# Kernel tuning notes

Measured on AMD Instinct MI355X. Metric: run time of the kernel, lower is better.

## Reference

```python
import jax, jax.numpy as jnp
import numpy as np
from jax import lax

T = 8  # primary_vec_length


def setup_inputs() -> dict:
    key = jax.random.key(0)
    k1, k2, k3 = jax.random.split(key, 3)
    x = jax.random.normal(k1, (32, 256, 64, 64), dtype=jnp.float32)
    # Conv2d weight [out_ch, in_ch, kH, kW], kaiming-ish scale
    W = jax.random.normal(k2, (32, 256, 9, 9), dtype=jnp.float32) * 0.01
    b = jax.random.normal(k3, (32,), dtype=jnp.float32) * 0.01
    return {"x": x, "W": W, "b": b}


def reference(x, W, b):
    B = x.shape[0]
    # Conv2d(kernel=9, stride=2, valid). The original applies this conv T times
    # to identical stacked copies of x; compute it once and broadcast (same math).
    conv = lax.conv_general_dilated(
        x, W, window_strides=(2, 2), padding="VALID",
        dimension_numbers=("NCHW", "OIHW", "NCHW"))
    conv = conv + b[None, :, None, None]            # [B, C, H', W']
    s = jnp.broadcast_to(conv[:, None], (B, T) + conv.shape[1:])  # [B, T, C, H', W']
    # squash along dim=1 (the capsule-vector / time dim)
    sq = jnp.sum(s * s, axis=1, keepdims=True)      # [B, 1, C, H', W']
    scale = sq / (1.0 + sq) / jnp.sqrt(sq + 1e-8)
    squ = s * scale                                  # [B, T, C, H', W']
    squ = squ.reshape(B, T, -1)                      # [B, T, C*H'*W']
    squ = jnp.transpose(squ, (0, 2, 1))[..., None]   # [B, N, T, 1]
    return squ
```

## Files before the change

### kernel.cpp

```cpp
#include <hip/hip_runtime.h>
#include <hip/hip_bf16.h>
#include <stdint.h>

typedef _Float16 f16;
typedef _Float16 f16x8 __attribute__((ext_vector_type(8)));
typedef float f32x16 __attribute__((ext_vector_type(16)));
typedef float f32x4 __attribute__((ext_vector_type(4)));
typedef uint32_t u32x4 __attribute__((ext_vector_type(4)));
typedef uint32_t u32x2 __attribute__((ext_vector_type(2)));

#define MFMA(A, B, C) __builtin_amdgcn_mfma_f32_32x32x16_f16((A), (B), (C), 0, 0, 0)

__global__ __launch_bounds__(256) void nchw_to_nhwc_f16(
    const float* __restrict__ x, f16* __restrict__ xt) {
  __shared__ __align__(16) uint32_t tile[64 * 128];
  const int bh = blockIdx.x;
  const int t = threadIdx.x;
  const float* src = x + (size_t)(bh >> 6) * (256 * 4096) + (bh & 63) * 64;

  const int w4 = t & 15;
  const int cq = t >> 4;
  const int xorv = 4 * (w4 & 7);
#pragma unroll
  for (int it = 0; it < 4; ++it) {
    const int c0 = it * 64 + cq * 4;
    float4 v0 = *(const float4*)(src + (size_t)(c0 + 0) * 4096 + w4 * 4);
    float4 v1 = *(const float4*)(src + (size_t)(c0 + 1) * 4096 + w4 * 4);
    float4 v2 = *(const float4*)(src + (size_t)(c0 + 2) * 4096 + w4 * 4);
    float4 v3 = *(const float4*)(src + (size_t)(c0 + 3) * 4096 + w4 * 4);
    const float* p0 = (const float*)&v0;
    const float* p1 = (const float*)&v1;
    const float* p2 = (const float*)&v2;
    const float* p3 = (const float*)&v3;
    const int u = it * 32 + cq * 2;
#pragma unroll
    for (int jw = 0; jw < 4; ++jw) {
      f16 h0 = (f16)p0[jw], h1 = (f16)p1[jw], h2 = (f16)p2[jw], h3 = (f16)p3[jw];
      uint32_t lo = (uint32_t)__builtin_bit_cast(uint16_t, h0) |
                    ((uint32_t)__builtin_bit_cast(uint16_t, h1) << 16);
      uint32_t hi = (uint32_t)__builtin_bit_cast(uint16_t, h2) |
                    ((uint32_t)__builtin_bit_cast(uint16_t, h3) << 16);
      u32x2 pk = {lo, hi};
      const int w = w4 * 4 + jw;
      *(u32x2*)&tile[w * 128 + (u ^ xorv)] = pk;
    }
  }
  __syncthreads();
  f16* dstb = xt + (size_t)bh * 16384;
#pragma unroll
  for (int it = 0; it < 8; ++it) {
    const int n = it * 256 + t;
    const int w2 = n & 31;
    const int par = (n >> 5) & 1;
    const int g8 = n >> 6;
    const int w = par + 2 * w2;
    const u32x4 v = *(const u32x4*)&tile[w * 128 + ((g8 * 4) ^ (4 * ((w >> 2) & 7)))];
    *(u32x4*)(dstb + n * 8) = v;
  }
}

__global__ __launch_bounds__(256) void pack_w(const float* __restrict__ W,
                                              f16* __restrict__ wt) {
  __shared__ float lds[10368];
  const int t = threadIdx.x;
  const int co = blockIdx.x >> 1;
  const int cih = blockIdx.x & 1;
  const float* src = W + (size_t)(co * 256 + cih * 128) * 81;
  for (int i = t; i < 10368; i += 256) lds[i] = src[i];
  __syncthreads();
  for (int j = t; j < 1296; j += 256) {
    const int kk = j >> 4;
    const int t16 = j & 15;
    const int cicl = t16 >> 2;
    const int sg = t16 & 3;
    const int cin = ((sg >> 1) & 1) * 16 + (sg & 1) * 8;
    f16 tmp[8];
#pragma unroll
    for (int e = 0; e < 8; ++e)
      tmp[e] = (f16)lds[(cicl * 32 + cin + e) * 81 + kk];
    const int cic = cih * 4 + cicl;
    *(f16x8*)&wt[(size_t)(((kk * 8 + cic) * 4 + sg) * 32 + co) * 8] = *(f16x8*)tmp;
  }
}

__global__ __launch_bounds__(256, 2) void conv_direct(
    const f16* __restrict__ xt, const f16* __restrict__ wt,
    float* __restrict__ convp) {
  __shared__ __align__(16) char stg[4 * 18432];
  const int tid = threadIdx.x;
  const int lane = tid & 63;
  const int wave = tid >> 6;
  const int m = lane & 31;
  const int hh = lane >> 5;

  const int blk = blockIdx.x;
  const int xcd = blk & 7;
  const int r = blk >> 3;
  const int i4 = r >> 4;
  const int rr = r & 15;
  const int og = rr >> 3;
  const int cic = rr & 7;
  const int bimg = xcd * 4 + i4;

  const int ohpA = og * 8 + wave;
  const int ohpB = ohpA + 4;
  const bool actB = (ohpB < 14);
  const int ohpBc = actB ? ohpB : ohpA;

  const char* xb = (const char*)xt;
  const char* wb = (const char*)wt;

  const char* ab0 = xb + ((size_t)(bimg * 64 + 4 * ohpA) * 32768 +
                          cic * 4096 + hh * 1024 + m * 16);
  const char* ab1 = xb + ((size_t)(bimg * 64 + 4 * ohpBc) * 32768 +
                          cic * 4096 + hh * 1024 + m * 16);
  const size_t cic2048 = (size_t)cic * 2048;
  const int fragoff = hh * 512 + m * 16;

#define GLDS(G, L)                                                            \
  __builtin_amdgcn_global_load_lds(                                           \
      (const __attribute__((address_space(1))) void*)(G),                     \
      (__attribute__((address_space(3))) void*)(L), 16, 0, 0)

#define ALOAD(AB, KW, P) \
  (*(const f16x8*)((AB) + (P) * 2048 + ((KW) & 1) * 512 + ((KW) >> 1) * 16))
#define LDSF(P) (*(const f16x8*)(P))

#define STAGE(JN)                                                             \
  {                                                                           \
    const int kkb = (JN) * 9;                                                 \
    char* db = stg + ((JN) & 3) * 18432;                                      \
    _Pragma("unroll") for (int i = 0; i < 4; ++i) {                           \
      const int u = tid + 256 * i;                                            \
      GLDS(wb + (size_t)(kkb + (u >> 7)) * 16384 + cic2048 + (u & 127) * 16,  \
           db + u * 16);                                                      \
    }                                                                         \
    if (tid < 128) {                                                          \
      GLDS(wb + (size_t)(kkb + 8) * 16384 + cic2048 + tid * 16,               \
           db + 16384 + tid * 16);                                            \
    }                                                                         \
  }

  f32x16 accA0, accA1, accB0, accB1;
#pragma unroll
  for (int i = 0; i < 16; ++i) {
    accA0[i] = 0.f; accA1[i] = 0.f; accB0[i] = 0.f; accB1[i] = 0.f;
  }

  STAGE(0)

  for (int j = 0; j < 11; ++j) {
    __syncthreads();
    if (j < 8) STAGE(j + 1)
    const char* s0 = stg + (j & 3) * 18432 + fragoff;
    const char* s1 = stg + ((j + 2) & 3) * 18432 + fragoff;
    f16x8 a00 = ALOAD(ab0, 0, 0), a01 = ALOAD(ab0, 0, 1);
    f16x8 a10 = ALOAD(ab1, 0, 0), a11 = ALOAD(ab1, 0, 1);
    if (j >= 2 && j <= 8) {
#pragma unroll
      for (int kw = 0; kw < 9; ++kw) {
        f16x8 n00, n01, n10, n11;
        if (kw < 8) {
          n00 = ALOAD(ab0, kw + 1, 0); n01 = ALOAD(ab0, kw + 1, 1);
          n10 = ALOAD(ab1, kw + 1, 0); n11 = ALOAD(ab1, kw + 1, 1);
        }
        const f16x8 b00 = LDSF(s0 + kw * 2048);
        const f16x8 b01 = LDSF(s0 + kw * 2048 + 1024);
        const f16x8 b10 = LDSF(s1 + kw * 2048);
        const f16x8 b11 = LDSF(s1 + kw * 2048 + 1024);
        accA0 = MFMA(a00, b00, accA0); accA0 = MFMA(a01, b01, accA0);
        accB0 = MFMA(a10, b00, accB0); accB0 = MFMA(a11, b01, accB0);
        accA1 = MFMA(a00, b10, accA1); accA1 = MFMA(a01, b11, accA1);
        accB1 = MFMA(a10, b10, accB1); accB1 = MFMA(a11, b11, accB1);
        a00 = n00; a01 = n01; a10 = n10; a11 = n11;
      }
    } else if (j < 2) {
#pragma unroll
      for (int kw = 0; kw < 9; ++kw) {
        f16x8 n00, n01, n10, n11;
        if (kw < 8) {
          n00 = ALOAD(ab0, kw + 1, 0); n01 = ALOAD(ab0, kw + 1, 1);
          n10 = ALOAD(ab1, kw + 1, 0); n11 = ALOAD(ab1, kw + 1, 1);
        }
        const f16x8 b00 = LDSF(s0 + kw * 2048);
        const f16x8 b01 = LDSF(s0 + kw * 2048 + 1024);
        accA0 = MFMA(a00, b00, accA0); accA0 = MFMA(a01, b01, accA0);
        accB0 = MFMA(a10, b00, accB0); accB0 = MFMA(a11, b01, accB0);
        a00 = n00; a01 = n01; a10 = n10; a11 = n11;
      }
    } else {
#pragma unroll
      for (int kw = 0; kw < 9; ++kw) {
        f16x8 n00, n01, n10, n11;
        if (kw < 8) {
          n00 = ALOAD(ab0, kw + 1, 0); n01 = ALOAD(ab0, kw + 1, 1);
          n10 = ALOAD(ab1, kw + 1, 0); n11 = ALOAD(ab1, kw + 1, 1);
        }
        const f16x8 b10 = LDSF(s1 + kw * 2048);
        const f16x8 b11 = LDSF(s1 + kw * 2048 + 1024);
        accA1 = MFMA(a00, b10, accA1); accA1 = MFMA(a01, b11, accA1);
        accB1 = MFMA(a10, b10, accB1); accB1 = MFMA(a11, b11, accB1);
        a00 = n00; a01 = n01; a10 = n10; a11 = n11;
      }
    }
    ab0 += 32768;
    ab1 += 32768;
  }
#undef STAGE
#undef ALOAD
#undef LDSF
#undef GLDS

#define STORE_PAIR(PP, ACT, A0, A1)                                           \
  if (ACT) {                                                                  \
    _Pragma("unroll") for (int tile = 0; tile < 2; ++tile) {                  \
      const int oh = 2 * (PP) + tile;                                         \
      float* cp = convp + (size_t)cic * 802816 +                              \
                  ((size_t)bimg * 784 + oh * 28) * 32 + m;                    \
      const f32x16& a = tile ? (A1) : (A0);                                   \
      _Pragma("unroll") for (int rI = 0; rI < 16; ++rI) {                     \
        const int ow = (rI & 3) + 8 * (rI >> 2) + 4 * hh;                     \
        if (ow < 28) cp[ow * 32] = a[rI];                                     \
      }                                                                       \
    }                                                                         \
  }
  STORE_PAIR(ohpA, true, accA0, accA1)
  STORE_PAIR(ohpB, actB, accB0, accB1)
#undef STORE_PAIR
}

__global__ __launch_bounds__(256) void epilogue(const float* __restrict__ convp,
                                                const float* __restrict__ bias,
                                                float* __restrict__ out) {
  const int gi = blockIdx.x * 256 + threadIdx.x;
  const int base = gi * 8;
  const int p = gi >> 2;
  const int co0 = (gi & 3) * 8;
  const int bi = p / 784;
  const int pix = p - bi * 784;
  f32x4 v0 = {0.f, 0.f, 0.f, 0.f}, v1 = {0.f, 0.f, 0.f, 0.f};
#pragma unroll
  for (int qq = 0; qq < 8; ++qq) {
    v0 += *(const f32x4*)&convp[(size_t)qq * 802816 + base];
    v1 += *(const f32x4*)&convp[(size_t)qq * 802816 + base + 4];
  }
  float vb[8];
#pragma unroll
  for (int jj = 0; jj < 4; ++jj) {
    vb[jj] = v0[jj] + bias[co0 + jj];
    vb[4 + jj] = v1[jj] + bias[co0 + 4 + jj];
  }
  float* ob = out + (size_t)bi * 200704 + pix * 8;
#pragma unroll
  for (int jj = 0; jj < 8; ++jj) {
    const float vv = vb[jj];
    const float sq = 8.f * vv * vv;
    const float scale = sq / ((1.f + sq) * sqrtf(sq + 1e-8f));
    const float y = vv * scale;
    const f32x4 qv = {y, y, y, y};
    float* o = ob + (size_t)(co0 + jj) * 6272;
    *(f32x4*)o = qv;
    *(f32x4*)(o + 4) = qv;
  }
}

extern "C" void kernel_launch(void* const* d_in, const int* in_sizes, int n_in,
                              void* d_out, int out_size, void* d_ws,
                              size_t ws_size, hipStream_t stream) {
  const float* x = (const float*)d_in[0];
  const float* W = (const float*)d_in[1];
  const float* bias = (const float*)d_in[2];
  float* out = (float*)d_out;

  char* ws = (char*)d_ws;
  f16* xt = (f16*)ws;
  f16* wt = (f16*)(ws + 67108864);
  float* convp = (float*)(ws + 67108864 + 1327104);

  nchw_to_nhwc_f16<<<dim3(2048), dim3(256), 0, stream>>>(x, xt);
  pack_w<<<dim3(64), dim3(256), 0, stream>>>(W, wt);
  conv_direct<<<dim3(512), dim3(256), 0, stream>>>(xt, wt, convp);
  epilogue<<<dim3(392), dim3(256), 0, stream>>>(convp, bias, out);
}
```

Measured before the change: 282.5 us.

## Split conv reduction into 16 partial slices with 512-thread blocks

The conv kernel's channel reduction is split twice as finely: each block now covers one image and half of a 32-channel chunk, and uses 8 waves to cover all output row pairs. Each wave issues one MFMA per weight fragment instead of two, and the per-stage LDS buffer halves so more blocks can be resident. The intent is more waves in flight to hide memory latency. In exchange, the partial-sum buffer doubles to 16 slices, so the epilogue reads twice as much data and the workspace grows. The tighter launch bounds of 512 threads with 4 blocks also risk register pressure and spills.

```diff
diff --git a/kernel.cpp b/kernel.cpp
--- a/kernel.cpp
+++ b/kernel.cpp
@@ -83,10 +83,10 @@
   }
 }
 
-__global__ __launch_bounds__(256, 2) void conv_direct(
+__global__ __launch_bounds__(512, 4) void conv_direct(
     const f16* __restrict__ xt, const f16* __restrict__ wt,
     float* __restrict__ convp) {
-  __shared__ __align__(16) char stg[4 * 18432];
+  __shared__ __align__(16) char stg[4 * 9216];
   const int tid = threadIdx.x;
   const int lane = tid & 63;
   const int wave = tid >> 6;
@@ -96,14 +96,14 @@
   const int blk = blockIdx.x;
   const int xcd = blk & 7;
   const int r = blk >> 3;
-  const int i4 = r >> 4;
-  const int rr = r & 15;
-  const int og = rr >> 3;
-  const int cic = rr & 7;
+  const int k16 = r >> 2;
+  const int i4 = r & 3;
   const int bimg = xcd * 4 + i4;
-
-  const int ohpA = og * 8 + wave;
-  const int ohpB = ohpA + 4;
+  const int cic = k16 >> 1;
+  const int sp = k16 & 1;
+
+  const int ohpA = wave;
+  const int ohpB = wave + 8;
   const bool actB = (ohpB < 14);
   const int ohpBc = actB ? ohpB : ohpA;
 
@@ -111,10 +111,10 @@
   const char* wb = (const char*)wt;
 
   const char* ab0 = xb + ((size_t)(bimg * 64 + 4 * ohpA) * 32768 +
-                          cic * 4096 + hh * 1024 + m * 16);
+                          cic * 4096 + sp * 2048 + hh * 1024 + m * 16);
   const char* ab1 = xb + ((size_t)(bimg * 64 + 4 * ohpBc) * 32768 +
-                          cic * 4096 + hh * 1024 + m * 16);
-  const size_t cic2048 = (size_t)cic * 2048;
+                          cic * 4096 + sp * 2048 + hh * 1024 + m * 16);
+  const size_t soff = (size_t)cic * 2048 + sp * 1024;
   const int fragoff = hh * 512 + m * 16;
 
 #define GLDS(G, L)                                                            \
@@ -122,22 +122,19 @@
       (const __attribute__((address_space(1))) void*)(G),                     \
       (__attribute__((address_space(3))) void*)(L), 16, 0, 0)
 
-#define ALOAD(AB, KW, P) \
-  (*(const f16x8*)((AB) + (P) * 2048 + ((KW) & 1) * 512 + ((KW) >> 1) * 16))
+#define ALOAD(AB, KW) \
+  (*(const f16x8*)((AB) + ((KW) & 1) * 512 + ((KW) >> 1) * 16))
 #define LDSF(P) (*(const f16x8*)(P))
 
 #define STAGE(JN)                                                             \
   {                                                                           \
     const int kkb = (JN) * 9;                                                 \
-    char* db = stg + ((JN) & 3) * 18432;                                      \
-    _Pragma("unroll") for (int i = 0; i < 4; ++i) {                           \
-      const int u = tid + 256 * i;                                            \
-      GLDS(wb + (size_t)(kkb + (u >> 7)) * 16384 + cic2048 + (u & 127) * 16,  \
-           db + u * 16);                                                      \
-    }                                                                         \
-    if (tid < 128) {                                                          \
-      GLDS(wb + (size_t)(kkb + 8) * 16384 + cic2048 + tid * 16,               \
-           db + 16384 + tid * 16);                                            \
+    char* db = stg + ((JN) & 3) * 9216;                                       \
+    GLDS(wb + (size_t)(kkb + (tid >> 6)) * 16384 + soff + (tid & 63) * 16,    \
+         db + tid * 16);                                                      \
+    if (tid < 64) {                                                           \
+      GLDS(wb + (size_t)(kkb + 8) * 16384 + soff + tid * 16,                  \
+           db + 8192 + tid * 16);                                             \
     }                                                                         \
   }
 
@@ -152,55 +149,42 @@
   for (int j = 0; j < 11; ++j) {
     __syncthreads();
     if (j < 8) STAGE(j + 1)
-    const char* s0 = stg + (j & 3) * 18432 + fragoff;
-    const char* s1 = stg + ((j + 2) & 3) * 18432 + fragoff;
-    f16x8 a00 = ALOAD(ab0, 0, 0), a01 = ALOAD(ab0, 0, 1);
-    f16x8 a10 = ALOAD(ab1, 0, 0), a11 = ALOAD(ab1, 0, 1);
+    const char* s0 = stg + (j & 3) * 9216 + fragoff;
+    const char* s1 = stg + ((j + 2) & 3) * 9216 + fragoff;
+    f16x8 a0 = ALOAD(ab0, 0);
+    f16x8 a1 = ALOAD(ab1, 0);
     if (j >= 2 && j <= 8) {
 #pragma unroll
       for (int kw = 0; kw < 9; ++kw) {
-        f16x8 n00, n01, n10, n11;
-        if (kw < 8) {
-          n00 = ALOAD(ab0, kw + 1, 0); n01 = ALOAD(ab0, kw + 1, 1);
-          n10 = ALOAD(ab1, kw + 1, 0); n11 = ALOAD(ab1, kw + 1, 1);
-        }
-        const f16x8 b00 = LDSF(s0 + kw * 2048);
-        const f16x8 b01 = LDSF(s0 + kw * 2048 + 1024);
-        const f16x8 b10 = LDSF(s1 + kw * 2048);
-        const f16x8 b11 = LDSF(s1 + kw * 2048 + 1024);
-        accA0 = MFMA(a00, b00, accA0); accA0 = MFMA(a01, b01, accA0);
-        accB0 = MFMA(a10, b00, accB0); accB0 = MFMA(a11, b01, accB0);
-        accA1 = MFMA(a00, b10, accA1); accA1 = MFMA(a01, b11, accA1);
-        accB1 = MFMA(a10, b10, accB1); accB1 = MFMA(a11, b11, accB1);
-        a00 = n00; a01 = n01; a10 = n10; a11 = n11;
+        f16x8 n0, n1;
+        if (kw < 8) { n0 = ALOAD(ab0, kw + 1); n1 = ALOAD(ab1, kw + 1); }
+        const f16x8 b0 = LDSF(s0 + kw * 1024);
+        const f16x8 b1 = LDSF(s1 + kw * 1024);
+        accA0 = MFMA(a0, b0, accA0);
+        accB0 = MFMA(a1, b0, accB0);
+        accA1 = MFMA(a0, b1, accA1);
+        accB1 = MFMA(a1, b1, accB1);
+        a0 = n0; a1 = n1;
       }
     } else if (j < 2) {
 #pragma unroll
       for (int kw = 0; kw < 9; ++kw) {
-        f16x8 n00, n01, n10, n11;
-        if (kw < 8) {
-          n00 = ALOAD(ab0, kw + 1, 0); n01 = ALOAD(ab0, kw + 1, 1);
-          n10 = ALOAD(ab1, kw + 1, 0); n11 = ALOAD(ab1, kw + 1, 1);
-        }
-        const f16x8 b00 = LDSF(s0 + kw * 2048);
-        const f16x8 b01 = LDSF(s0 + kw * 2048 + 1024);
-        accA0 = MFMA(a00, b00, accA0); accA0 = MFMA(a01, b01, accA0);
-        accB0 = MFMA(a10, b00, accB0); accB0 = MFMA(a11, b01, accB0);
-        a00 = n00; a01 = n01; a10 = n10; a11 = n11;
+        f16x8 n0, n1;
+        if (kw < 8) { n0 = ALOAD(ab0, kw + 1); n1 = ALOAD(ab1, kw + 1); }
+        const f16x8 b0 = LDSF(s0 + kw * 1024);
+        accA0 = MFMA(a0, b0, accA0);
+        accB0 = MFMA(a1, b0, accB0);
+        a0 = n0; a1 = n1;
       }
     } else {
 #pragma unroll
       for (int kw = 0; kw < 9; ++kw) {
-        f16x8 n00, n01, n10, n11;
-        if (kw < 8) {
-          n00 = ALOAD(ab0, kw + 1, 0); n01 = ALOAD(ab0, kw + 1, 1);
-          n10 = ALOAD(ab1, kw + 1, 0); n11 = ALOAD(ab1, kw + 1, 1);
-        }
-        const f16x8 b10 = LDSF(s1 + kw * 2048);
-        const f16x8 b11 = LDSF(s1 + kw * 2048 + 1024);
-        accA1 = MFMA(a00, b10, accA1); accA1 = MFMA(a01, b11, accA1);
-        accB1 = MFMA(a10, b10, accB1); accB1 = MFMA(a11, b11, accB1);
-        a00 = n00; a01 = n01; a10 = n10; a11 = n11;
+        f16x8 n0, n1;
+        if (kw < 8) { n0 = ALOAD(ab0, kw + 1); n1 = ALOAD(ab1, kw + 1); }
+        const f16x8 b1 = LDSF(s1 + kw * 1024);
+        accA1 = MFMA(a0, b1, accA1);
+        accB1 = MFMA(a1, b1, accB1);
+        a0 = n0; a1 = n1;
       }
     }
     ab0 += 32768;
@@ -215,7 +199,7 @@
   if (ACT) {                                                                  \
     _Pragma("unroll") for (int tile = 0; tile < 2; ++tile) {                  \
       const int oh = 2 * (PP) + tile;                                         \
-      float* cp = convp + (size_t)cic * 802816 +                              \
+      float* cp = convp + (size_t)k16 * 802816 +                              \
                   ((size_t)bimg * 784 + oh * 28) * 32 + m;                    \
       const f32x16& a = tile ? (A1) : (A0);                                   \
       _Pragma("unroll") for (int rI = 0; rI < 16; ++rI) {                     \
@@ -240,7 +224,7 @@
   const int pix = p - bi * 784;
   f32x4 v0 = {0.f, 0.f, 0.f, 0.f}, v1 = {0.f, 0.f, 0.f, 0.f};
 #pragma unroll
-  for (int qq = 0; qq < 8; ++qq) {
+  for (int qq = 0; qq < 16; ++qq) {
     v0 += *(const f32x4*)&convp[(size_t)qq * 802816 + base];
     v1 += *(const f32x4*)&convp[(size_t)qq * 802816 + base + 4];
   }
@@ -279,6 +263,6 @@
 
   nchw_to_nhwc_f16<<<dim3(2048), dim3(256), 0, stream>>>(x, xt);
   pack_w<<<dim3(64), dim3(256), 0, stream>>>(W, wt);
-  conv_direct<<<dim3(512), dim3(256), 0, stream>>>(xt, wt, convp);
+  conv_direct<<<dim3(512), dim3(512), 0, stream>>>(xt, wt, convp);
   epilogue<<<dim3(392), dim3(256), 0, stream>>>(convp, bias, out);
 }
```

New measurement: 281.9 us. About the same (-0.2%).
